# Kernel optimization log

Hardware: AMD Instinct MI355X
Metric: run time of the kernel (lower is better)

The kernel has to match this reference:

```python
import jax, jax.numpy as jnp
import numpy as np

D_MODEL = 1024
N_HEADS = 16
HEAD_DIM = D_MODEL // N_HEADS


def setup_inputs() -> dict:
    key = jax.random.key(0)
    k1, k2, k3 = jax.random.split(key, 3)
    B, T = 4, 2048
    x = jax.random.normal(k1, (B, T, D_MODEL), dtype=jnp.float32)
    # match nn.Linear default init scale roughly (small weights for stability)
    w_qkv = jax.random.normal(k2, (D_MODEL, 3 * D_MODEL), dtype=jnp.float32) / np.sqrt(D_MODEL)
    w_proj = jax.random.normal(k3, (D_MODEL, D_MODEL), dtype=jnp.float32) / np.sqrt(D_MODEL)
    b_proj = jnp.zeros((D_MODEL,), dtype=jnp.float32)
    return {"x": x, "w_qkv": w_qkv, "w_proj": w_proj, "b_proj": b_proj}


def reference(x, w_qkv, w_proj, b_proj):
    B, T, C = x.shape
    qkv = x @ w_qkv  # [B,T,3C]
    q, k, v = jnp.split(qkv, 3, axis=-1)
    # [B, H, T, hd]
    q = q.reshape(B, T, N_HEADS, HEAD_DIM).transpose(0, 2, 1, 3)
    k = k.reshape(B, T, N_HEADS, HEAD_DIM).transpose(0, 2, 1, 3)
    v = v.reshape(B, T, N_HEADS, HEAD_DIM).transpose(0, 2, 1, 3)
    scale = 1.0 / np.sqrt(HEAD_DIM).astype(np.float32)
    att = jnp.einsum("bhqd,bhkd->bhqk", q, k) * scale
    causal = jnp.tril(jnp.ones((T, T), dtype=bool))
    att = jnp.where(causal[None, None], att, jnp.float32(-jnp.inf))
    att = jax.nn.softmax(att, axis=-1)
    # dropout p=0.0 (eval) -> identity
    out = jnp.einsum("bhqk,bhkd->bhqd", att, v)
    out = out.transpose(0, 2, 1, 3).reshape(B, T, C)
    return out @ w_proj + b_proj
```

## Files before the change

### kernel.cpp

```cpp
#include <hip/hip_runtime.h>
#include <stdint.h>

#define D_MODEL 1024
#define N_HEADS 16
#define HEAD_DIM 64
#define BATCH 4
#define SEQ 2048
#define ROWS (BATCH * SEQ)
#define K3 (3 * D_MODEL)
#define NQT (SEQ / 64)
#define SCALE_Q 0.1803368867f

typedef unsigned short u16;
typedef unsigned int u32;
typedef __attribute__((ext_vector_type(8))) short short8;
typedef __attribute__((ext_vector_type(4))) float floatx4;

typedef const __attribute__((address_space(1))) u32* gptr_t;
typedef __attribute__((address_space(3))) u32* lptr_t;

__device__ __forceinline__ float bf2f(u16 u) {
    return __uint_as_float(((unsigned)u) << 16);
}
__device__ __forceinline__ u16 f2b(float f) {
    unsigned u = __float_as_uint(f);
    u = u + 0x7fffu + ((u >> 16) & 1u);
    return (u16)(u >> 16);
}
__device__ __forceinline__ unsigned pk2(float a, float b) {
    return (unsigned)f2b(a) | ((unsigned)f2b(b) << 16);
}

__global__ __launch_bounds__(256) void conv_f2b4(const float* __restrict__ x,
                                                 u16* __restrict__ xb, int n4) {
    int i = blockIdx.x * 256 + threadIdx.x;
    if (i < n4) {
        float4 v = ((const float4*)x)[i];
        uint2 p;
        p.x = pk2(v.x, v.y);
        p.y = pk2(v.z, v.w);
        ((uint2*)xb)[i] = p;
    }
}

__global__ __launch_bounds__(256) void transpose_f2b_t(const float* __restrict__ w,
                                                       u16* __restrict__ wt,
                                                       int R, int C) {
    __shared__ u16 tile[64][65];
    const int tx = threadIdx.x & 63;
    const int ty = threadIdx.x >> 6;
    const int r0 = blockIdx.y * 64, c0 = blockIdx.x * 64;
    #pragma unroll
    for (int i = 0; i < 16; ++i) {
        const int r = i * 4 + ty;
        tile[r][tx] = f2b(w[(size_t)(r0 + r) * C + c0 + tx]);
    }
    __syncthreads();
    #pragma unroll
    for (int i = 0; i < 16; ++i) {
        const int c = i * 4 + ty;
        wt[(size_t)(c0 + c) * R + r0 + tx] = tile[tx][c];
    }
}

__global__ __launch_bounds__(256) void transpose_v2(const u16* __restrict__ v,
                                                    u16* __restrict__ vt) {
    __shared__ u16 tile[64][65];
    const int bh = blockIdx.y;
    const int t0 = blockIdx.x * 64;
    const int tx = threadIdx.x & 63, ty = threadIdx.x >> 6;
    const u16* src = v + ((size_t)bh * SEQ + t0) * HEAD_DIM;
    #pragma unroll
    for (int i = 0; i < 16; ++i) {
        const int r = i * 4 + ty;
        tile[r][tx] = src[r * HEAD_DIM + tx];
    }
    __syncthreads();
    u16* dst = vt + (size_t)bh * HEAD_DIM * SEQ + t0;
    #pragma unroll
    for (int i = 0; i < 16; ++i) {
        const int d = i * 4 + ty;
        dst[(size_t)d * SEQ + tx] = tile[tx][d];
    }
}

#define GEMM_CORE_GLD(KDIM)                                                    \
    __shared__ u16 As[128][64];                                                \
    __shared__ u16 Bs[128][64];                                                \
    const int tid  = threadIdx.x;                                              \
    const int wave = tid >> 6, lane = tid & 63;                                \
    const int quad = lane >> 4, l15 = lane & 15;                               \
    const int wr = wave >> 1, wc = wave & 1;                                   \
    const int m0 = blockIdx.y * 128, n0 = blockIdx.x * 128;                    \
    const int lrow8 = lane >> 3;                                               \
    const int csw = 8 * ((lane & 7) ^ lrow8);           \
    const int swA = (l15 & 7) * 8;                      \
    floatx4 acc[4][4] = {};                                                    \
    for (int k0 = 0; k0 < (KDIM); k0 += 64) {                                  \
        _Pragma("unroll")                                                      \
        for (int i = 0; i < 4; ++i) {                                          \
            const int rb = i * 32 + wave * 8;                                  \
            const int r  = rb + lrow8;                                         \
            __builtin_amdgcn_global_load_lds(                                  \
                (gptr_t)(A + (size_t)(m0 + r) * (KDIM) + k0 + csw),            \
                (lptr_t)(&As[rb][0]), 16, 0, 0);                               \
            __builtin_amdgcn_global_load_lds(                                  \
                (gptr_t)(Bt + (size_t)(n0 + r) * (KDIM) + k0 + csw),           \
                (lptr_t)(&Bs[rb][0]), 16, 0, 0);                               \
        }                                                                      \
        __syncthreads();                                                       \
        _Pragma("unroll")                                                      \
        for (int ks = 0; ks < 2; ++ks) {                                       \
            const int kk = ks * 32 + quad * 8;                                 \
            short8 af[4], bf[4];                                               \
            _Pragma("unroll")                                                  \
            for (int t = 0; t < 4; ++t) {                                      \
                af[t] = *(const short8*)&As[wr * 64 + t * 16 + l15][kk ^ swA]; \
                bf[t] = *(const short8*)&Bs[wc * 64 + t * 16 + l15][kk ^ swA]; \
            }                                                                  \
            _Pragma("unroll")                                                  \
            for (int i = 0; i < 4; ++i)                                        \
                _Pragma("unroll")                                              \
                for (int j = 0; j < 4; ++j)                                    \
                    acc[i][j] = __builtin_amdgcn_mfma_f32_16x16x32_bf16(       \
                        af[i], bf[j], acc[i][j], 0, 0, 0);                     \
        }                                                                      \
        __syncthreads();                                                       \
    }

__global__ __launch_bounds__(256) void gemm_qkv(const u16* __restrict__ A,
                                                const u16* __restrict__ Bt,
                                                u16* __restrict__ qo,
                                                u16* __restrict__ ko,
                                                u16* __restrict__ vo) {
    GEMM_CORE_GLD(D_MODEL)
    const int which = n0 >> 10;
    u16* dst = which == 0 ? qo : (which == 1 ? ko : vo);
    const float scl = which == 0 ? SCALE_Q : 1.f;
    #pragma unroll
    for (int i = 0; i < 4; ++i)
        #pragma unroll
        for (int j = 0; j < 4; ++j) {
            const int col = n0 + wc * 64 + j * 16 + l15;
            const int rb  = m0 + wr * 64 + i * 16 + quad * 4;
            const int cc  = col & 1023;
            const int h = cc >> 6, d = cc & 63;
            #pragma unroll
            for (int rr = 0; rr < 4; ++rr) {
                const int row = rb + rr;
                const int b = row >> 11, t = row & 2047;
                dst[(((size_t)(b * N_HEADS + h)) * SEQ + t) * HEAD_DIM + d] =
                    f2b(acc[i][j][rr] * scl);
            }
        }
}

__global__ __launch_bounds__(256) void gemm_proj(const u16* __restrict__ A,
                                                 const u16* __restrict__ Bt,
                                                 const float* __restrict__ bias,
                                                 float* __restrict__ out) {
    GEMM_CORE_GLD(D_MODEL)
    #pragma unroll
    for (int i = 0; i < 4; ++i)
        #pragma unroll
        for (int j = 0; j < 4; ++j) {
            const int col = n0 + wc * 64 + j * 16 + l15;
            const int rb  = m0 + wr * 64 + i * 16 + quad * 4;
            const float bv = bias[col];
            #pragma unroll
            for (int rr = 0; rr < 4; ++rr) {
                const int row = rb + rr;
                out[(size_t)row * D_MODEL + col] = acc[i][j][rr] + bv;
            }
        }
}

__global__ __launch_bounds__(256, 4) void attn_mfma(const u16* __restrict__ q,
                                                    const u16* __restrict__ k,
                                                    const u16* __restrict__ vt,
                                                    u16* __restrict__ o) {
    __shared__ u16 Ks[2][64][64];
    __shared__ u16 Vs[2][64][64];
    __shared__ u16 Plds[4][16][64];
    const int tid = threadIdx.x;
    const int w = tid >> 6, lane = tid & 63;
    const int quad = lane >> 4, l15 = lane & 15;
    const int bh = blockIdx.y;
    const int b = bh >> 4, h = bh & 15;
    const u16* kb  = k  + (size_t)bh * SEQ * HEAD_DIM;
    const u16* vtb = vt + (size_t)bh * HEAD_DIM * SEQ;
    const int lrow8 = lane >> 3;
    const int csw = 8 * ((lane & 7) ^ lrow8);
    const int swA = (l15 & 7) * 8;
    const int r0 = w * 16 + lrow8;

    #pragma unroll 1
    for (int seg = 0; seg < 2; ++seg) {
        const int qt = seg ? (int)blockIdx.x : (NQT - 1 - (int)blockIdx.x);
        const int qrow = qt * 64 + w * 16 + l15;
        const u16* qp = q + ((size_t)bh * SEQ + qrow) * HEAD_DIM + quad * 8;
        const short8 bq0 = *(const short8*)(qp);
        const short8 bq1 = *(const short8*)(qp + 32);

        floatx4 O[4] = {};
        float l = 0.f;

        __syncthreads();
        __builtin_amdgcn_global_load_lds(
            (gptr_t)(kb + (size_t)(r0) * HEAD_DIM + csw),
            (lptr_t)(&Ks[0][w * 16][0]), 16, 0, 0);
        __builtin_amdgcn_global_load_lds(
            (gptr_t)(kb + (size_t)(r0 + 8) * HEAD_DIM + csw),
            (lptr_t)(&Ks[0][w * 16 + 8][0]), 16, 0, 0);
        __builtin_amdgcn_global_load_lds(
            (gptr_t)(vtb + (size_t)(r0) * SEQ + csw),
            (lptr_t)(&Vs[0][w * 16][0]), 16, 0, 0);
        __builtin_amdgcn_global_load_lds(
            (gptr_t)(vtb + (size_t)(r0 + 8) * SEQ + csw),
            (lptr_t)(&Vs[0][w * 16 + 8][0]), 16, 0, 0);

        for (int c = 0; c <= qt; ++c) {
            const int cb = c & 1;
            __syncthreads();
            if (c < qt) {
                const int nb = cb ^ 1;
                __builtin_amdgcn_global_load_lds(
                    (gptr_t)(kb + (size_t)((c + 1) * 64 + r0) * HEAD_DIM + csw),
                    (lptr_t)(&Ks[nb][w * 16][0]), 16, 0, 0);
                __builtin_amdgcn_global_load_lds(
                    (gptr_t)(kb + (size_t)((c + 1) * 64 + r0 + 8) * HEAD_DIM + csw),
                    (lptr_t)(&Ks[nb][w * 16 + 8][0]), 16, 0, 0);
                __builtin_amdgcn_global_load_lds(
                    (gptr_t)(vtb + (size_t)(r0) * SEQ + (c + 1) * 64 + csw),
                    (lptr_t)(&Vs[nb][w * 16][0]), 16, 0, 0);
                __builtin_amdgcn_global_load_lds(
                    (gptr_t)(vtb + (size_t)(r0 + 8) * SEQ + (c + 1) * 64 + csw),
                    (lptr_t)(&Vs[nb][w * 16 + 8][0]), 16, 0, 0);
            }
            floatx4 s[4];
            #pragma unroll
            for (int kt = 0; kt < 4; ++kt) {
                short8 ak0 = *(const short8*)&Ks[cb][kt * 16 + l15][(quad * 8) ^ swA];
                short8 ak1 = *(const short8*)&Ks[cb][kt * 16 + l15][(32 + quad * 8) ^ swA];
                floatx4 z = {};
                z = __builtin_amdgcn_mfma_f32_16x16x32_bf16(ak0, bq0, z, 0, 0, 0);
                z = __builtin_amdgcn_mfma_f32_16x16x32_bf16(ak1, bq1, z, 0, 0, 0);
                s[kt] = z;
            }
            float e[4][4];
            #pragma unroll
            for (int kt = 0; kt < 4; ++kt)
                #pragma unroll
                for (int r = 0; r < 4; ++r)
                    e[kt][r] = exp2f(s[kt][r]);
            if (c == qt) {
                #pragma unroll
                for (int kt = 0; kt < 4; ++kt)
                    #pragma unroll
                    for (int r = 0; r < 4; ++r)
                        if (kt * 16 + quad * 4 + r > w * 16 + l15) e[kt][r] = 0.f;
            }
            float ls = 0.f;
            #pragma unroll
            for (int kt = 0; kt < 4; ++kt) {
                ls += (e[kt][0] + e[kt][1]) + (e[kt][2] + e[kt][3]);
                uint2 pkv;
                pkv.x = pk2(e[kt][0], e[kt][1]);
                pkv.y = pk2(e[kt][2], e[kt][3]);
                *(uint2*)&Plds[w][l15][(kt * 16 + quad * 4) ^ swA] = pkv;
            }
            l += ls;
            short8 pb0 = *(const short8*)&Plds[w][l15][(quad * 8) ^ swA];
            short8 pb1 = *(const short8*)&Plds[w][l15][(32 + quad * 8) ^ swA];
            #pragma unroll
            for (int dt = 0; dt < 4; ++dt) {
                short8 av0 = *(const short8*)&Vs[cb][dt * 16 + l15][(quad * 8) ^ swA];
                short8 av1 = *(const short8*)&Vs[cb][dt * 16 + l15][(32 + quad * 8) ^ swA];
                O[dt] = __builtin_amdgcn_mfma_f32_16x16x32_bf16(av0, pb0, O[dt], 0, 0, 0);
                O[dt] = __builtin_amdgcn_mfma_f32_16x16x32_bf16(av1, pb1, O[dt], 0, 0, 0);
            }
        }
        l += __shfl_xor(l, 16);
        l += __shfl_xor(l, 32);
        const float inv = 1.f / l;
        u16* op = o + ((size_t)(b * SEQ + qrow)) * D_MODEL + h * 64 + quad * 4;
        #pragma unroll
        for (int dt = 0; dt < 4; ++dt) {
            uint2 pkv;
            pkv.x = pk2(O[dt][0] * inv, O[dt][1] * inv);
            pkv.y = pk2(O[dt][2] * inv, O[dt][3] * inv);
            *(uint2*)(op + dt * 16) = pkv;
        }
    }
}

extern "C" void kernel_launch(void* const* d_in, const int* in_sizes, int n_in,
                              void* d_out, int out_size, void* d_ws, size_t ws_size,
                              hipStream_t stream) {
    const float* x      = (const float*)d_in[0];
    const float* w_qkv  = (const float*)d_in[1];
    const float* w_proj = (const float*)d_in[2];
    const float* b_proj = (const float*)d_in[3];
    float* out = (float*)d_out;

    u16* xb      = (u16*)d_ws;
    u16* wt_qkv  = xb + (size_t)ROWS * D_MODEL;
    u16* wt_proj = wt_qkv + (size_t)D_MODEL * K3;
    u16* qws     = wt_proj + (size_t)D_MODEL * D_MODEL;
    u16* kws     = qws + (size_t)ROWS * D_MODEL;
    u16* vtws    = kws + (size_t)ROWS * D_MODEL;
    u16* aout    = vtws + (size_t)ROWS * D_MODEL;
    u16* vnat    = aout;

    conv_f2b4<<<(ROWS * D_MODEL / 4 + 255) / 256, 256, 0, stream>>>(x, xb, ROWS * D_MODEL / 4);
    transpose_f2b_t<<<dim3(K3 / 64, D_MODEL / 64), 256, 0, stream>>>(w_qkv, wt_qkv, D_MODEL, K3);
    transpose_f2b_t<<<dim3(D_MODEL / 64, D_MODEL / 64), 256, 0, stream>>>(w_proj, wt_proj, D_MODEL, D_MODEL);

    gemm_qkv<<<dim3(K3 / 128, ROWS / 128), 256, 0, stream>>>(xb, wt_qkv, qws, kws, vnat);

    transpose_v2<<<dim3(SEQ / 64, BATCH * N_HEADS), 256, 0, stream>>>(vnat, vtws);

    attn_mfma<<<dim3(NQT / 2, BATCH * N_HEADS), 256, 0, stream>>>(qws, kws, vtws, aout);

    gemm_proj<<<dim3(D_MODEL / 128, ROWS / 128), 256, 0, stream>>>(aout, wt_proj, b_proj, out);
}
```

Baseline: 271.3 us.

## Use hardware bf16 pack, XCD-aware block swizzle, and MFMA row-sum in attention

Replaces the software round-to-nearest bf16 conversion with the v_cvt_pk_bf16_f32 instruction in every kernel. Remaps workgroup IDs in both GEMMs and in the attention kernel so that consecutive tiles land on the same XCD, which should improve L2 reuse. In attention, the softmax denominator is now accumulated with an extra MFMA against a ones vector, applied to the bf16-rounded probabilities, replacing the scalar sums and cross-lane shuffles. This adds two MFMAs per key tile. The denominator now matches the bf16 P used in P·V, which slightly changes the numerics.

After: 254.6 us. -6.2%, faster.

```diff
diff --git a/kernel.cpp b/kernel.cpp
--- a/kernel.cpp
+++ b/kernel.cpp
@@ -19,16 +19,10 @@
 typedef const __attribute__((address_space(1))) u32* gptr_t;
 typedef __attribute__((address_space(3))) u32* lptr_t;
 
-__device__ __forceinline__ float bf2f(u16 u) {
-    return __uint_as_float(((unsigned)u) << 16);
-}
-__device__ __forceinline__ u16 f2b(float f) {
-    unsigned u = __float_as_uint(f);
-    u = u + 0x7fffu + ((u >> 16) & 1u);
-    return (u16)(u >> 16);
-}
-__device__ __forceinline__ unsigned pk2(float a, float b) {
-    return (unsigned)f2b(a) | ((unsigned)f2b(b) << 16);
+__device__ __forceinline__ unsigned cvt_pk(float lo, float hi) {
+    unsigned r;
+    asm("v_cvt_pk_bf16_f32 %0, %1, %2" : "=v"(r) : "v"(lo), "v"(hi));
+    return r;
 }
 
 __global__ __launch_bounds__(256) void conv_f2b4(const float* __restrict__ x,
@@ -37,8 +31,8 @@
     if (i < n4) {
         float4 v = ((const float4*)x)[i];
         uint2 p;
-        p.x = pk2(v.x, v.y);
-        p.y = pk2(v.z, v.w);
+        p.x = cvt_pk(v.x, v.y);
+        p.y = cvt_pk(v.z, v.w);
         ((uint2*)xb)[i] = p;
     }
 }
@@ -51,9 +45,12 @@
     const int ty = threadIdx.x >> 6;
     const int r0 = blockIdx.y * 64, c0 = blockIdx.x * 64;
     #pragma unroll
-    for (int i = 0; i < 16; ++i) {
-        const int r = i * 4 + ty;
-        tile[r][tx] = f2b(w[(size_t)(r0 + r) * C + c0 + tx]);
+    for (int i = 0; i < 16; i += 2) {
+        const float a = w[(size_t)(r0 + i * 4 + ty) * C + c0 + tx];
+        const float b = w[(size_t)(r0 + (i + 1) * 4 + ty) * C + c0 + tx];
+        const unsigned p = cvt_pk(a, b);
+        tile[i * 4 + ty][tx] = (u16)p;
+        tile[(i + 1) * 4 + ty][tx] = (u16)(p >> 16);
     }
     __syncthreads();
     #pragma unroll
@@ -84,14 +81,17 @@
     }
 }
 
-#define GEMM_CORE_GLD(KDIM)                                                    \
+#define GEMM_CORE_GLD(KDIM, NXB)                                               \
     __shared__ u16 As[128][64];                                                \
     __shared__ u16 Bs[128][64];                                                \
     const int tid  = threadIdx.x;                                              \
     const int wave = tid >> 6, lane = tid & 63;                                \
     const int quad = lane >> 4, l15 = lane & 15;                               \
     const int wr = wave >> 1, wc = wave & 1;                                   \
-    const int m0 = blockIdx.y * 128, n0 = blockIdx.x * 128;                    \
+    const int bid = (int)(blockIdx.y * gridDim.x + blockIdx.x);                \
+    const int nwg = (int)(gridDim.x * gridDim.y);                              \
+    const int swz = (bid & 7) * (nwg >> 3) + (bid >> 3);      \
+    const int m0 = (swz / (NXB)) * 128, n0 = (swz % (NXB)) * 128;              \
     const int lrow8 = lane >> 3;                                               \
     const int csw = 8 * ((lane & 7) ^ lrow8);           \
     const int swA = (l15 & 7) * 8;                      \
@@ -133,7 +133,7 @@
                                                 u16* __restrict__ qo,
                                                 u16* __restrict__ ko,
                                                 u16* __restrict__ vo) {
-    GEMM_CORE_GLD(D_MODEL)
+    GEMM_CORE_GLD(D_MODEL, 24)
     const int which = n0 >> 10;
     u16* dst = which == 0 ? qo : (which == 1 ? ko : vo);
     const float scl = which == 0 ? SCALE_Q : 1.f;
@@ -146,11 +146,17 @@
             const int cc  = col & 1023;
             const int h = cc >> 6, d = cc & 63;
             #pragma unroll
-            for (int rr = 0; rr < 4; ++rr) {
-                const int row = rb + rr;
-                const int b = row >> 11, t = row & 2047;
-                dst[(((size_t)(b * N_HEADS + h)) * SEQ + t) * HEAD_DIM + d] =
-                    f2b(acc[i][j][rr] * scl);
+            for (int rr = 0; rr < 4; rr += 2) {
+                const unsigned pw = cvt_pk(acc[i][j][rr] * scl,
+                                           acc[i][j][rr + 1] * scl);
+                int row = rb + rr;
+                int b_ = row >> 11, t_ = row & 2047;
+                dst[(((size_t)(b_ * N_HEADS + h)) * SEQ + t_) * HEAD_DIM + d] =
+                    (u16)pw;
+                row = rb + rr + 1;
+                b_ = row >> 11; t_ = row & 2047;
+                dst[(((size_t)(b_ * N_HEADS + h)) * SEQ + t_) * HEAD_DIM + d] =
+                    (u16)(pw >> 16);
             }
         }
 }
@@ -159,7 +165,7 @@
                                                  const u16* __restrict__ Bt,
                                                  const float* __restrict__ bias,
                                                  float* __restrict__ out) {
-    GEMM_CORE_GLD(D_MODEL)
+    GEMM_CORE_GLD(D_MODEL, 8)
     #pragma unroll
     for (int i = 0; i < 4; ++i)
         #pragma unroll
@@ -185,7 +191,10 @@
     const int tid = threadIdx.x;
     const int w = tid >> 6, lane = tid & 63;
     const int quad = lane >> 4, l15 = lane & 15;
-    const int bh = blockIdx.y;
+    const int bid = (int)(blockIdx.y * 16 + blockIdx.x);
+    const int swzb = (bid & 7) * 128 + (bid >> 3);
+    const int bh = swzb >> 4;
+    const int qx = swzb & 15;
     const int b = bh >> 4, h = bh & 15;
     const u16* kb  = k  + (size_t)bh * SEQ * HEAD_DIM;
     const u16* vtb = vt + (size_t)bh * HEAD_DIM * SEQ;
@@ -193,17 +202,19 @@
     const int csw = 8 * ((lane & 7) ^ lrow8);
     const int swA = (l15 & 7) * 8;
     const int r0 = w * 16 + lrow8;
+    const short8 ones = {0x3F80, 0x3F80, 0x3F80, 0x3F80,
+                         0x3F80, 0x3F80, 0x3F80, 0x3F80};
 
     #pragma unroll 1
     for (int seg = 0; seg < 2; ++seg) {
-        const int qt = seg ? (int)blockIdx.x : (NQT - 1 - (int)blockIdx.x);
+        const int qt = seg ? qx : (NQT - 1 - qx);
         const int qrow = qt * 64 + w * 16 + l15;
         const u16* qp = q + ((size_t)bh * SEQ + qrow) * HEAD_DIM + quad * 8;
         const short8 bq0 = *(const short8*)(qp);
         const short8 bq1 = *(const short8*)(qp + 32);
 
         floatx4 O[4] = {};
-        float l = 0.f;
+        floatx4 Lacc = {};
 
         __syncthreads();
         __builtin_amdgcn_global_load_lds(
@@ -260,16 +271,13 @@
                     for (int r = 0; r < 4; ++r)
                         if (kt * 16 + quad * 4 + r > w * 16 + l15) e[kt][r] = 0.f;
             }
-            float ls = 0.f;
             #pragma unroll
             for (int kt = 0; kt < 4; ++kt) {
-                ls += (e[kt][0] + e[kt][1]) + (e[kt][2] + e[kt][3]);
                 uint2 pkv;
-                pkv.x = pk2(e[kt][0], e[kt][1]);
-                pkv.y = pk2(e[kt][2], e[kt][3]);
+                pkv.x = cvt_pk(e[kt][0], e[kt][1]);
+                pkv.y = cvt_pk(e[kt][2], e[kt][3]);
                 *(uint2*)&Plds[w][l15][(kt * 16 + quad * 4) ^ swA] = pkv;
             }
-            l += ls;
             short8 pb0 = *(const short8*)&Plds[w][l15][(quad * 8) ^ swA];
             short8 pb1 = *(const short8*)&Plds[w][l15][(32 + quad * 8) ^ swA];
             #pragma unroll
@@ -279,16 +287,16 @@
                 O[dt] = __builtin_amdgcn_mfma_f32_16x16x32_bf16(av0, pb0, O[dt], 0, 0, 0);
                 O[dt] = __builtin_amdgcn_mfma_f32_16x16x32_bf16(av1, pb1, O[dt], 0, 0, 0);
             }
+            Lacc = __builtin_amdgcn_mfma_f32_16x16x32_bf16(ones, pb0, Lacc, 0, 0, 0);
+            Lacc = __builtin_amdgcn_mfma_f32_16x16x32_bf16(ones, pb1, Lacc, 0, 0, 0);
         }
-        l += __shfl_xor(l, 16);
-        l += __shfl_xor(l, 32);
-        const float inv = 1.f / l;
+        const float inv = 1.f / Lacc[0];
         u16* op = o + ((size_t)(b * SEQ + qrow)) * D_MODEL + h * 64 + quad * 4;
         #pragma unroll
         for (int dt = 0; dt < 4; ++dt) {
             uint2 pkv;
-            pkv.x = pk2(O[dt][0] * inv, O[dt][1] * inv);
-            pkv.y = pk2(O[dt][2] * inv, O[dt][3] * inv);
+            pkv.x = cvt_pk(O[dt][0] * inv, O[dt][1] * inv);
+            pkv.y = cvt_pk(O[dt][2] * inv, O[dt][3] * inv);
             *(uint2*)(op + dt * 16) = pkv;
         }
     }
```
